# Performance work log

Measured on AMD Instinct MI355X. Metric: run time of the kernel, lower is better.

The kernel has to match this reference:

```python
import jax, jax.numpy as jnp
import numpy as np

N = 50000      # nodes per graph
E = 1600000    # edges per graph
D_IN = 128
D_HID = 128
D_OUT = 128
D_GF = 128
N_LAYERS = 3   # input->hid, hid->hid (hidden_layer=1), hid->out


def setup_inputs() -> dict:
    key = jax.random.key(0)
    ks = jax.random.split(key, 24)
    inp = {
        "feat_p": jax.random.normal(ks[0], (N, D_IN), jnp.float32),
        "src_p": jax.random.randint(ks[1], (E,), 0, N, jnp.int32),
        "dst_p": jax.random.randint(ks[2], (E,), 0, N, jnp.int32),
        "feat_s": jax.random.normal(ks[3], (N, D_IN), jnp.float32),
        "src_s": jax.random.randint(ks[4], (E,), 0, N, jnp.int32),
        "dst_s": jax.random.randint(ks[5], (E,), 0, N, jnp.int32),
    }
    dims = [(D_IN, D_HID), (D_HID, D_HID), (D_HID, D_OUT)]
    for i, (di, do) in enumerate(dims):
        inp[f"W{i}"] = jax.random.normal(ks[6 + 2 * i], (di, do), jnp.float32) * 0.05
        inp[f"b{i}"] = jnp.zeros((do,), jnp.float32)
    inp["Wr"] = jax.random.normal(ks[14], (D_OUT, D_GF), jnp.float32) * 0.05
    inp["br"] = jnp.zeros((D_GF,), jnp.float32)
    inp["Wm1"] = jax.random.normal(ks[15], (2 * D_GF, D_GF), jnp.float32) * 0.05
    inp["bm1"] = jnp.zeros((D_GF,), jnp.float32)
    inp["Wm2"] = jax.random.normal(ks[16], (D_GF, 1), jnp.float32) * 0.05
    inp["bm2"] = jnp.zeros((1,), jnp.float32)
    return inp


def _gcn_stack(feat, src, dst, layers):
    """Stacked GCN: mean over incoming messages, then linear.
    NOTE: the original SingleGCN never applies its ReLU (bug preserved)."""
    n = feat.shape[0]
    deg = jax.ops.segment_sum(jnp.ones_like(src, feat.dtype), dst, num_segments=n)
    inv_deg = (1.0 / jnp.maximum(deg, 1.0))[:, None]  # [N,1]
    h = feat
    for W, b in layers:
        msg = h[src]                                           # [E,d] gather
        agg = jax.ops.segment_sum(msg, dst, num_segments=n)    # [N,d] scatter-add
        h = (agg * inv_deg) @ W + b                            # mean + linear
    return h


def reference(feat_p, src_p, dst_p, feat_s, src_s, dst_s,
              W0, b0, W1, b1, W2, b2, Wr, br, Wm1, bm1, Wm2, bm2):
    layers = [(W0, b0), (W1, b1), (W2, b2)]
    h_p = _gcn_stack(feat_p, src_p, dst_p, layers)
    h_s = _gcn_stack(feat_s, src_s, dst_s, layers)
    # ReadOut: mean over nodes -> linear -> sigmoid
    g_p = jax.nn.sigmoid(jnp.mean(h_p, axis=0) @ Wr + br)  # [D_GF]
    g_s = jax.nn.sigmoid(jnp.mean(h_s, axis=0) @ Wr + br)
    # Match: concat -> linear -> linear -> sigmoid
    c = jnp.concatenate([g_p, g_s], axis=-1)               # [2*D_GF]
    d = (c @ Wm1 + bm1) @ Wm2 + bm2                        # [1]
    return jax.nn.sigmoid(d)
```

## Files before the change

### kernel.cpp

```cpp
#include <hip/hip_runtime.h>
#include <math.h>

#define D 128
#define BSH 9
#define NPB 512
#define SLOT 128
#define STCAP 6252
#define NBB 256
#define NBKT_MAX 128


__global__ __launch_bounds__(512) void bin_kernel(
        const int* __restrict__ src_p, const int* __restrict__ dst_p,
        const int* __restrict__ src_s, const int* __restrict__ dst_s,
        int* __restrict__ sbins, unsigned short* __restrict__ dbins,
        unsigned* __restrict__ cnt_s, unsigned* __restrict__ cnt_d,
        int E, int nbkt) {
    const int g = blockIdx.y, b = blockIdx.x;
    const int* src = g ? src_s : src_p;
    const int* dst = g ? dst_s : dst_p;
    int* sb = sbins + (size_t)g * nbkt * NBB * SLOT;
    unsigned short* db = dbins + (size_t)g * nbkt * NBB * SLOT;
    unsigned* csp = cnt_s + (size_t)g * nbkt * NBB;
    unsigned* cdp = cnt_d + (size_t)g * nbkt * NBB;

    __shared__ int sstage[STCAP];
    __shared__ unsigned short dstage[STCAP];
    __shared__ unsigned hist_s[NBKT_MAX], hist_d[NBKT_MAX];
    __shared__ unsigned offs_s[NBKT_MAX], offs_d[NBKT_MAX];
    __shared__ unsigned lcur_s[NBKT_MAX], lcur_d[NBKT_MAX];

    const int tid = threadIdx.x;
    const int wv = tid >> 6, lane = tid & 63;
    for (int i = tid; i < NBKT_MAX; i += 512) { hist_s[i] = 0u; hist_d[i] = 0u; }
    __syncthreads();

    const int e0 = b * STCAP;
    const int e1 = min(e0 + STCAP, E);
    const int efull = e0 + ((e1 - e0) & ~3);

    for (int e = e0 + tid * 4; e + 4 <= e1; e += 512 * 4) {
        int4 s4 = *(const int4*)(src + e);
        int4 d4 = *(const int4*)(dst + e);
        atomicAdd(&hist_s[s4.x >> BSH], 1u);
        atomicAdd(&hist_s[s4.y >> BSH], 1u);
        atomicAdd(&hist_s[s4.z >> BSH], 1u);
        atomicAdd(&hist_s[s4.w >> BSH], 1u);
        atomicAdd(&hist_d[d4.x >> BSH], 1u);
        atomicAdd(&hist_d[d4.y >> BSH], 1u);
        atomicAdd(&hist_d[d4.z >> BSH], 1u);
        atomicAdd(&hist_d[d4.w >> BSH], 1u);
    }
    for (int e = efull + tid; e < e1; e += 512) {
        atomicAdd(&hist_s[src[e] >> BSH], 1u);
        atomicAdd(&hist_d[dst[e] >> BSH], 1u);
    }
    __syncthreads();

    if (wv == 0 || wv == 1) {
        const unsigned* h = (wv == 0) ? hist_s : hist_d;
        unsigned* o = (wv == 0) ? offs_s : offs_d;
        unsigned* lc = (wv == 0) ? lcur_s : lcur_d;
        unsigned a = (2 * lane < nbkt) ? h[2 * lane] : 0u;
        unsigned bb = (2 * lane + 1 < nbkt) ? h[2 * lane + 1] : 0u;
        unsigned v = a + bb;
        for (int d2 = 1; d2 < 64; d2 <<= 1) {
            unsigned t = __shfl_up(v, d2);
            if (lane >= d2) v += t;
        }
        unsigned ex = v - (a + bb);
        if (2 * lane < nbkt) { o[2 * lane] = ex; lc[2 * lane] = ex; }
        if (2 * lane + 1 < nbkt) { o[2 * lane + 1] = ex + a; lc[2 * lane + 1] = ex + a; }
    }
    __syncthreads();

    for (int e = e0 + tid * 4; e + 4 <= e1; e += 512 * 4) {
        int4 s4 = *(const int4*)(src + e);
        int4 d4 = *(const int4*)(dst + e);
        int sv[4] = {s4.x, s4.y, s4.z, s4.w};
        int dv[4] = {d4.x, d4.y, d4.z, d4.w};
        #pragma unroll
        for (int k = 0; k < 4; ++k) {
            unsigned p = atomicAdd(&lcur_s[sv[k] >> BSH], 1u);
            sstage[p] = ((sv[k] & (NPB - 1)) << 17) | dv[k];
            unsigned pd = atomicAdd(&lcur_d[dv[k] >> BSH], 1u);
            dstage[pd] = (unsigned short)(dv[k] & (NPB - 1));
        }
    }
    for (int e = efull + tid; e < e1; e += 512) {
        int s = src[e], d2 = dst[e];
        unsigned p = atomicAdd(&lcur_s[s >> BSH], 1u);
        sstage[p] = ((s & (NPB - 1)) << 17) | d2;
        unsigned pd = atomicAdd(&lcur_d[d2 >> BSH], 1u);
        dstage[pd] = (unsigned short)(d2 & (NPB - 1));
    }
    __syncthreads();

    for (int q = wv; q < nbkt; q += 8) {
        unsigned cs = min(hist_s[q], (unsigned)SLOT);
        unsigned os = offs_s[q];
        int* dp = sb + ((size_t)q * NBB + b) * SLOT;
        for (unsigned i = lane; i < cs; i += 64) dp[i] = sstage[os + i];
        unsigned cd = min(hist_d[q], (unsigned)SLOT);
        unsigned od = offs_d[q];
        unsigned short* ddp = db + ((size_t)q * NBB + b) * SLOT;
        for (unsigned i = lane; i < cd; i += 64) ddp[i] = dstage[od + i];
        if (lane == 0) { csp[q * NBB + b] = cs; cdp[q * NBB + b] = cd; }
    }
}

__global__ __launch_bounds__(512) void deg_inv(
        const unsigned short* __restrict__ dbins, const unsigned* __restrict__ cnt_d,
        float* __restrict__ inv, float* __restrict__ zbase, int zcount,
        int N, int nbkt) {
    const int q = blockIdx.x, g = blockIdx.y;
    const int tid = threadIdx.x, wv = tid >> 6;
    if (q == 0 && g == 0)
        for (int i = tid; i < zcount; i += 512) zbase[i] = 0.f;
    const unsigned short* dq = dbins + ((size_t)g * nbkt + q) * NBB * SLOT;
    const unsigned* cq = cnt_d + (size_t)g * nbkt * NBB + (size_t)q * NBB;
    __shared__ float bl[8][NPB];
    __shared__ unsigned lcnt[NBB];
    if (tid < NBB) lcnt[tid] = cq[tid];
    for (int i = tid; i < 8 * NPB; i += 512) ((float*)bl)[i] = 0.f;
    __syncthreads();
    float* mybl = bl[wv];
    const ushort4* d4 = (const ushort4*)dq;
    for (int i = tid; i < NBB * (SLOT / 4); i += 512) {
        int lim = (int)lcnt[i >> 5] - ((i & 31) << 2);
        if (lim <= 0) continue;
        ushort4 v = d4[i];
        atomicAdd(&mybl[v.x], 1.f);
        if (lim > 1) atomicAdd(&mybl[v.y], 1.f);
        if (lim > 2) atomicAdd(&mybl[v.z], 1.f);
        if (lim > 3) atomicAdd(&mybl[v.w], 1.f);
    }
    __syncthreads();
    float t = 0.f;
    #pragma unroll
    for (int r = 0; r < 8; ++r) t += bl[r][tid];
    int node = q * NPB + tid;
    if (node < N) inv[(size_t)g * N + node] = 1.0f / fmaxf(t, 1.0f);
}

__global__ __launch_bounds__(512) void prop_scan(
        const int* __restrict__ sbins, const unsigned* __restrict__ cnt_s,
        const float* __restrict__ w, const float* __restrict__ inv,
        float* __restrict__ out_w,
        const float* __restrict__ feat_p, const float* __restrict__ feat_s,
        float* __restrict__ fpart2, float* __restrict__ sums, int s_idx,
        int N, int nbkt, float scale) {
    const int q = blockIdx.x, g = blockIdx.y;
    const int* sq = sbins + ((size_t)g * nbkt + q) * NBB * SLOT;
    const unsigned* cq = cnt_s + (size_t)g * nbkt * NBB + (size_t)q * NBB;
    const float* wg = w + (size_t)g * N;
    const int tid = threadIdx.x, wv = tid >> 6;
    __shared__ float bl[8][NPB];
    __shared__ unsigned lcnt[NBB];
    __shared__ float red[NPB];
    if (tid < NBB) lcnt[tid] = cq[tid];
    for (int i = tid; i < 8 * NPB; i += 512) ((float*)bl)[i] = 0.f;
    __syncthreads();
    float* mybl = bl[wv];
    const int4* s4 = (const int4*)sq;
    for (int i = tid; i < NBB * (SLOT / 4); i += 512) {
        int lim = (int)lcnt[i >> 5] - ((i & 31) << 2);
        if (lim <= 0) continue;
        int4 v = s4[i];
        int iy = (lim > 1) ? (v.y & 0x1FFFF) : 0;
        int iz = (lim > 2) ? (v.z & 0x1FFFF) : 0;
        int iw = (lim > 3) ? (v.w & 0x1FFFF) : 0;
        float a = wg[v.x & 0x1FFFF];
        float b2 = wg[iy];
        float c2 = wg[iz];
        float d2 = wg[iw];
        atomicAdd(&mybl[((unsigned)v.x) >> 17], a);
        if (lim > 1) atomicAdd(&mybl[((unsigned)v.y) >> 17], b2);
        if (lim > 2) atomicAdd(&mybl[((unsigned)v.z) >> 17], c2);
        if (lim > 3) atomicAdd(&mybl[((unsigned)v.w) >> 17], d2);
    }
    __syncthreads();
    float t = 0.f;
    #pragma unroll
    for (int r = 0; r < 8; ++r) t += bl[r][tid];
    const float u = t * scale;
    const int node = q * NPB + tid;
    const bool valid = node < N;
    if (valid && out_w) {
        size_t off = (size_t)g * N + node;
        out_w[off] = u * inv[off];
    }
    if (sums) {
        red[tid] = valid ? u : 0.f;
        __syncthreads();
        for (int st = 256; st > 0; st >>= 1) {
            if (tid < st) red[tid] += red[tid + st];
            __syncthreads();
        }
        if (tid == 0 && red[0] != 0.f) atomicAdd(&sums[g * 2 + s_idx], red[0]);
    }
    if (fpart2) {
        red[tid] = valid ? u : 0.f;
        __syncthreads();
        const float* feat = g ? feat_s : feat_p;
        const int j = tid & 127, rg = tid >> 7;
        const int base = q * NPB;
        const int rmax = min(NPB, N - base);
        float acc = 0.f;
        const int rend = min((rg + 1) * 128, rmax);
        for (int r = rg * 128; r < rend; ++r)
            acc += red[r] * feat[(size_t)(base + r) * D + j];
        ((float*)bl)[rg * 128 + j] = acc;
        __syncthreads();
        if (rg == 0) {
            float tot = ((float*)bl)[j] + ((float*)bl)[128 + j] +
                        ((float*)bl)[256 + j] + ((float*)bl)[384 + j];
            atomicAdd(&fpart2[((size_t)g * 16 + (q & 15)) * D + j], tot);
        }
    }
}

__global__ __launch_bounds__(512) void final_kernel(
        const float* __restrict__ fpart2,
        const float* __restrict__ sums,
        const float* __restrict__ W0, const float* __restrict__ b0,
        const float* __restrict__ W1, const float* __restrict__ b1,
        const float* __restrict__ W2, const float* __restrict__ b2,
        const float* __restrict__ Wr, const float* __restrict__ br,
        const float* __restrict__ Wm1, const float* __restrict__ bm1,
        const float* __restrict__ Wm2, const float* __restrict__ bm2,
        float* __restrict__ out) {
    __shared__ float x[128];
    __shared__ float part[4][128];
    __shared__ float rvec[256];
    __shared__ float Avec[128], Bvec[128];
    __shared__ float gv[256];
    const int tid = threadIdx.x;
    const int j = tid & 127;
    const int h = tid >> 7;

    auto mv128 = [&](const float* __restrict__ W, float* __restrict__ buf) {
        float p = 0.f;
        const float* Wp = W + (size_t)(h * 32) * 128 + j;
        #pragma unroll
        for (int i = 0; i < 32; ++i) p += buf[h * 32 + i] * Wp[(size_t)i * 128];
        part[h][j] = p;
        __syncthreads();
        if (h == 0) buf[j] = part[0][j] + part[1][j] + part[2][j] + part[3][j];
        __syncthreads();
    };

    if (tid < 256) {
        int g = tid >> 7;
        const float* fp = fpart2 + (size_t)g * 2048 + (tid & 127);
        float rv = 0.f;
        #pragma unroll
        for (int b = 0; b < 16; ++b) rv += fp[(size_t)b * 128];
        rvec[tid] = rv;
    }
    __syncthreads();

    if (tid < 128) x[tid] = b0[tid];
    __syncthreads();
    mv128(W1, x);
    mv128(W2, x);
    if (tid < 128) Avec[tid] = x[tid];
    __syncthreads();
    if (tid < 128) x[tid] = b1[tid];
    __syncthreads();
    mv128(W2, x);
    if (tid < 128) Bvec[tid] = x[tid];
    __syncthreads();

    for (int g = 0; g < 2; ++g) {
        const float s1 = sums[g * 2 + 0];
        const float s2 = sums[g * 2 + 1];
        if (tid < 128) x[tid] = rvec[g * 128 + tid];
        __syncthreads();
        mv128(W0, x);
        mv128(W1, x);
        mv128(W2, x);
        if (tid < 128) x[tid] += s2 * Avec[tid] + s1 * Bvec[tid] + b2[tid];
        __syncthreads();
        mv128(Wr, x);
        if (tid < 128) gv[g * 128 + tid] = 1.0f / (1.0f + expf(-(x[tid] + br[tid])));
        __syncthreads();
    }

    {
        float p = 0.f;
        const float* Wp = Wm1 + (size_t)(h * 64) * 128 + j;
        #pragma unroll
        for (int i = 0; i < 64; ++i) p += gv[h * 64 + i] * Wp[(size_t)i * 128];
        part[h][j] = p;
        __syncthreads();
        if (h == 0)
            part[0][j] = (part[0][j] + part[1][j] + part[2][j] + part[3][j] + bm1[j]) * Wm2[j];
        __syncthreads();
        if (tid < 64) part[0][tid] += part[0][tid + 64];
        __syncthreads();
        if (tid < 32) part[0][tid] += part[0][tid + 32];
        __syncthreads();
        if (tid < 16) part[0][tid] += part[0][tid + 16];
        __syncthreads();
        if (tid < 8) part[0][tid] += part[0][tid + 8];
        __syncthreads();
        if (tid < 4) part[0][tid] += part[0][tid + 4];
        __syncthreads();
        if (tid < 2) part[0][tid] += part[0][tid + 2];
        __syncthreads();
        if (tid == 0) out[0] = 1.0f / (1.0f + expf(-(part[0][0] + part[0][1] + bm2[0])));
    }
}

extern "C" void kernel_launch(void* const* d_in, const int* in_sizes, int n_in,
                              void* d_out, int out_size, void* d_ws, size_t ws_size,
                              hipStream_t stream) {
    const float* feat_p = (const float*)d_in[0];
    const int*   src_p  = (const int*)d_in[1];
    const int*   dst_p  = (const int*)d_in[2];
    const float* feat_s = (const float*)d_in[3];
    const int*   src_s  = (const int*)d_in[4];
    const int*   dst_s  = (const int*)d_in[5];
    const float* W0 = (const float*)d_in[6];
    const float* b0 = (const float*)d_in[7];
    const float* W1 = (const float*)d_in[8];
    const float* b1 = (const float*)d_in[9];
    const float* W2 = (const float*)d_in[10];
    const float* b2 = (const float*)d_in[11];
    const float* Wr = (const float*)d_in[12];
    const float* br = (const float*)d_in[13];
    const float* Wm1 = (const float*)d_in[14];
    const float* bm1 = (const float*)d_in[15];
    const float* Wm2 = (const float*)d_in[16];
    const float* bm2 = (const float*)d_in[17];
    float* out = (float*)d_out;

    const int N = in_sizes[0] / D;
    const int E = in_sizes[1];
    const int N2 = 2 * N;
    const int nbkt = (N + NPB - 1) >> BSH;

    float* ws     = (float*)d_ws;
    float* sums   = ws;
    float* fpart2 = ws + 16;
    float* inv    = fpart2 + 2 * 16 * 128;
    float* w1     = inv + N2;
    float* w2     = w1 + N2;
    unsigned* cnt_s = (unsigned*)(w2 + N2);
    unsigned* cnt_d = cnt_s + (size_t)2 * nbkt * NBB;
    int* sbins    = (int*)(cnt_d + (size_t)2 * nbkt * NBB);
    unsigned short* dbins = (unsigned short*)(sbins + (size_t)2 * nbkt * NBB * SLOT);

    const float u0 = 1.0f / (float)N;
    const int zcount = 16 + 2 * 16 * 128;

    bin_kernel<<<dim3(NBB, 2), 512, 0, stream>>>(src_p, dst_p, src_s, dst_s,
                                                 sbins, dbins, cnt_s, cnt_d,
                                                 E, nbkt);

    deg_inv<<<dim3(nbkt, 2), 512, 0, stream>>>(dbins, cnt_d, inv, ws, zcount,
                                               N, nbkt);

    prop_scan<<<dim3(nbkt, 2), 512, 0, stream>>>(sbins, cnt_s, inv, inv, w1,
                                                 nullptr, nullptr, nullptr,
                                                 sums, 0, N, nbkt, u0);
    prop_scan<<<dim3(nbkt, 2), 512, 0, stream>>>(sbins, cnt_s, w1, inv, w2,
                                                 nullptr, nullptr, nullptr,
                                                 sums, 1, N, nbkt, 1.0f);
    prop_scan<<<dim3(nbkt, 2), 512, 0, stream>>>(sbins, cnt_s, w2, inv, nullptr,
                                                 feat_p, feat_s, fpart2,
                                                 nullptr, 0, N, nbkt, 1.0f);

    final_kernel<<<1, 512, 0, stream>>>(fpart2, sums, W0, b0, W1, b1, W2, b2,
                                        Wr, br, Wm1, bm1, Wm2, bm2, out);
}
```

Baseline: 317.2 us.

## Split per-bucket degree and propagation scans into sub-block partials plus combine kernels

The degree-count and scalar-propagation scans ran with only about 196 blocks (nbkt × 2). They are now split eight ways along the source-block dimension, giving about 1568 blocks of 256 threads. Each block writes per-node partial sums to a workspace buffer, and separate combine kernels sum the partials, apply inv-degree, reduce the sums and do the feature-weighted accumulation. The feature pass is now spread over twice as many blocks. This should fill the GPU's compute units better, at the cost of extra launches and partials traffic through global memory.

```diff
diff --git a/kernel.cpp b/kernel.cpp
--- a/kernel.cpp
+++ b/kernel.cpp
@@ -8,6 +8,8 @@
 #define STCAP 6252
 #define NBB 256
 #define NBKT_MAX 128
+#define SB 8
+#define CPS (NBB / SB)
 
 
 __global__ __launch_bounds__(512) void bin_kernel(
@@ -109,24 +111,22 @@
     }
 }
 
-__global__ __launch_bounds__(512) void deg_inv(
+__global__ __launch_bounds__(256) void deg_part(
         const unsigned short* __restrict__ dbins, const unsigned* __restrict__ cnt_d,
-        float* __restrict__ inv, float* __restrict__ zbase, int zcount,
-        int N, int nbkt) {
-    const int q = blockIdx.x, g = blockIdx.y;
+        float* __restrict__ partials, int nbkt) {
+    const int s = blockIdx.x, q = blockIdx.y, g = blockIdx.z;
+    const unsigned short* dq = dbins + ((size_t)(g * nbkt + q) * NBB + s * CPS) * SLOT;
+    const unsigned* cq = cnt_d + (size_t)(g * nbkt + q) * NBB + s * CPS;
     const int tid = threadIdx.x, wv = tid >> 6;
-    if (q == 0 && g == 0)
-        for (int i = tid; i < zcount; i += 512) zbase[i] = 0.f;
-    const unsigned short* dq = dbins + ((size_t)g * nbkt + q) * NBB * SLOT;
-    const unsigned* cq = cnt_d + (size_t)g * nbkt * NBB + (size_t)q * NBB;
-    __shared__ float bl[8][NPB];
-    __shared__ unsigned lcnt[NBB];
-    if (tid < NBB) lcnt[tid] = cq[tid];
-    for (int i = tid; i < 8 * NPB; i += 512) ((float*)bl)[i] = 0.f;
+    __shared__ float bl[4][NPB];
+    __shared__ unsigned lcnt[CPS];
+    if (tid < CPS) lcnt[tid] = cq[tid];
+    for (int i = tid; i < 4 * NPB; i += 256) ((float*)bl)[i] = 0.f;
     __syncthreads();
     float* mybl = bl[wv];
     const ushort4* d4 = (const ushort4*)dq;
-    for (int i = tid; i < NBB * (SLOT / 4); i += 512) {
+    const int total = CPS * (SLOT / 4);
+    for (int i = tid; i < total; i += 256) {
         int lim = (int)lcnt[i >> 5] - ((i & 31) << 2);
         if (lim <= 0) continue;
         ushort4 v = d4[i];
@@ -136,34 +136,44 @@
         if (lim > 3) atomicAdd(&mybl[v.w], 1.f);
     }
     __syncthreads();
+    float* pp = partials + (((size_t)(g * nbkt + q)) * SB + s) * NPB;
+    for (int i = tid; i < NPB; i += 256)
+        pp[i] = bl[0][i] + bl[1][i] + bl[2][i] + bl[3][i];
+}
+
+__global__ __launch_bounds__(512) void deg_combine(
+        const float* __restrict__ partials, float* __restrict__ inv,
+        float* __restrict__ zbase, int zcount, int N, int nbkt) {
+    const int q = blockIdx.x, g = blockIdx.y;
+    const int tid = threadIdx.x;
+    if (q == 0 && g == 0)
+        for (int i = tid; i < zcount; i += 512) zbase[i] = 0.f;
+    const float* pp = partials + ((size_t)(g * nbkt + q)) * SB * NPB;
     float t = 0.f;
     #pragma unroll
-    for (int r = 0; r < 8; ++r) t += bl[r][tid];
-    int node = q * NPB + tid;
+    for (int s = 0; s < SB; ++s) t += pp[s * NPB + tid];
+    const int node = q * NPB + tid;
     if (node < N) inv[(size_t)g * N + node] = 1.0f / fmaxf(t, 1.0f);
 }
 
-__global__ __launch_bounds__(512) void prop_scan(
+__global__ __launch_bounds__(256) void part_scan(
         const int* __restrict__ sbins, const unsigned* __restrict__ cnt_s,
-        const float* __restrict__ w, const float* __restrict__ inv,
-        float* __restrict__ out_w,
-        const float* __restrict__ feat_p, const float* __restrict__ feat_s,
-        float* __restrict__ fpart2, float* __restrict__ sums, int s_idx,
-        int N, int nbkt, float scale) {
-    const int q = blockIdx.x, g = blockIdx.y;
-    const int* sq = sbins + ((size_t)g * nbkt + q) * NBB * SLOT;
-    const unsigned* cq = cnt_s + (size_t)g * nbkt * NBB + (size_t)q * NBB;
+        const float* __restrict__ w, float* __restrict__ partials,
+        int N, int nbkt) {
+    const int s = blockIdx.x, q = blockIdx.y, g = blockIdx.z;
+    const int* sq = sbins + ((size_t)(g * nbkt + q) * NBB + s * CPS) * SLOT;
+    const unsigned* cq = cnt_s + (size_t)(g * nbkt + q) * NBB + s * CPS;
     const float* wg = w + (size_t)g * N;
     const int tid = threadIdx.x, wv = tid >> 6;
-    __shared__ float bl[8][NPB];
-    __shared__ unsigned lcnt[NBB];
-    __shared__ float red[NPB];
-    if (tid < NBB) lcnt[tid] = cq[tid];
-    for (int i = tid; i < 8 * NPB; i += 512) ((float*)bl)[i] = 0.f;
+    __shared__ float bl[4][NPB];
+    __shared__ unsigned lcnt[CPS];
+    if (tid < CPS) lcnt[tid] = cq[tid];
+    for (int i = tid; i < 4 * NPB; i += 256) ((float*)bl)[i] = 0.f;
     __syncthreads();
     float* mybl = bl[wv];
     const int4* s4 = (const int4*)sq;
-    for (int i = tid; i < NBB * (SLOT / 4); i += 512) {
+    const int total = CPS * (SLOT / 4);
+    for (int i = tid; i < total; i += 256) {
         int lim = (int)lcnt[i >> 5] - ((i & 31) << 2);
         if (lim <= 0) continue;
         int4 v = s4[i];
@@ -180,43 +190,70 @@
         if (lim > 3) atomicAdd(&mybl[((unsigned)v.w) >> 17], d2);
     }
     __syncthreads();
+    float* pp = partials + (((size_t)(g * nbkt + q)) * SB + s) * NPB;
+    for (int i = tid; i < NPB; i += 256)
+        pp[i] = bl[0][i] + bl[1][i] + bl[2][i] + bl[3][i];
+}
+
+__global__ __launch_bounds__(512) void prop_combine(
+        const float* __restrict__ partials, const float* __restrict__ inv,
+        float* __restrict__ out_w, float* __restrict__ sums, int s_idx,
+        int N, int nbkt, float scale) {
+    const int q = blockIdx.x, g = blockIdx.y;
+    const int tid = threadIdx.x;
+    const float* pp = partials + ((size_t)(g * nbkt + q)) * SB * NPB;
     float t = 0.f;
     #pragma unroll
-    for (int r = 0; r < 8; ++r) t += bl[r][tid];
+    for (int s = 0; s < SB; ++s) t += pp[s * NPB + tid];
     const float u = t * scale;
     const int node = q * NPB + tid;
     const bool valid = node < N;
-    if (valid && out_w) {
+    if (valid) {
         size_t off = (size_t)g * N + node;
         out_w[off] = u * inv[off];
     }
-    if (sums) {
-        red[tid] = valid ? u : 0.f;
-        __syncthreads();
-        for (int st = 256; st > 0; st >>= 1) {
-            if (tid < st) red[tid] += red[tid + st];
-            __syncthreads();
-        }
-        if (tid == 0 && red[0] != 0.f) atomicAdd(&sums[g * 2 + s_idx], red[0]);
-    }
-    if (fpart2) {
-        red[tid] = valid ? u : 0.f;
-        __syncthreads();
-        const float* feat = g ? feat_s : feat_p;
-        const int j = tid & 127, rg = tid >> 7;
-        const int base = q * NPB;
-        const int rmax = min(NPB, N - base);
-        float acc = 0.f;
-        const int rend = min((rg + 1) * 128, rmax);
-        for (int r = rg * 128; r < rend; ++r)
-            acc += red[r] * feat[(size_t)(base + r) * D + j];
-        ((float*)bl)[rg * 128 + j] = acc;
-        __syncthreads();
-        if (rg == 0) {
-            float tot = ((float*)bl)[j] + ((float*)bl)[128 + j] +
-                        ((float*)bl)[256 + j] + ((float*)bl)[384 + j];
+    __shared__ float red[NPB];
+    red[tid] = valid ? u : 0.f;
+    __syncthreads();
+    for (int st = 256; st > 0; st >>= 1) {
+        if (tid < st) red[tid] += red[tid + st];
+        __syncthreads();
+    }
+    if (tid == 0 && red[0] != 0.f) atomicAdd(&sums[g * 2 + s_idx], red[0]);
+}
+
+__global__ __launch_bounds__(512) void feat_combine(
+        const float* __restrict__ partials,
+        const float* __restrict__ feat_p, const float* __restrict__ feat_s,
+        float* __restrict__ fpart2, int N, int nbkt) {
+    const int r = blockIdx.x, q = blockIdx.y, g = blockIdx.z;
+    const int tid = threadIdx.x;
+    __shared__ float red[256];
+    __shared__ float accb[512];
+    const float* pp = partials + ((size_t)(g * nbkt + q)) * SB * NPB + r * 256;
+    const int base = q * NPB + r * 256;
+    if (tid < 256) {
+        float t = 0.f;
+        #pragma unroll
+        for (int s = 0; s < SB; ++s) t += pp[s * NPB + tid];
+        red[tid] = (base + tid < N) ? t : 0.f;
+    }
+    __syncthreads();
+    const float* feat = g ? feat_s : feat_p;
+    const int j = tid & 127, rg = tid >> 7;
+    int rmax = N - base;
+    rmax = (rmax < 0) ? 0 : ((rmax > 256) ? 256 : rmax);
+    const int rstart = rg * 64;
+    const int rend = min(rstart + 64, rmax);
+    float acc = 0.f;
+    for (int row = rstart; row < rend; ++row)
+        acc += red[row] * feat[(size_t)(base + row) * D + j];
+    accb[rg * 128 + j] = acc;
+    __syncthreads();
+    if (rg == 0) {
+        float tot = accb[j] + accb[128 + j] + accb[256 + j] + accb[384 + j];
+        if (tot != 0.f)
             atomicAdd(&fpart2[((size_t)g * 16 + (q & 15)) * D + j], tot);
-        }
     }
 }
 
@@ -347,7 +384,8 @@
     float* inv    = fpart2 + 2 * 16 * 128;
     float* w1     = inv + N2;
     float* w2     = w1 + N2;
-    unsigned* cnt_s = (unsigned*)(w2 + N2);
+    float* partials = w2 + N2;
+    unsigned* cnt_s = (unsigned*)(partials + (size_t)2 * nbkt * SB * NPB);
     unsigned* cnt_d = cnt_s + (size_t)2 * nbkt * NBB;
     int* sbins    = (int*)(cnt_d + (size_t)2 * nbkt * NBB);
     unsigned short* dbins = (unsigned short*)(sbins + (size_t)2 * nbkt * NBB * SLOT);
@@ -359,18 +397,24 @@
                                                  sbins, dbins, cnt_s, cnt_d,
                                                  E, nbkt);
 
-    deg_inv<<<dim3(nbkt, 2), 512, 0, stream>>>(dbins, cnt_d, inv, ws, zcount,
-                                               N, nbkt);
-
-    prop_scan<<<dim3(nbkt, 2), 512, 0, stream>>>(sbins, cnt_s, inv, inv, w1,
-                                                 nullptr, nullptr, nullptr,
-                                                 sums, 0, N, nbkt, u0);
-    prop_scan<<<dim3(nbkt, 2), 512, 0, stream>>>(sbins, cnt_s, w1, inv, w2,
-                                                 nullptr, nullptr, nullptr,
-                                                 sums, 1, N, nbkt, 1.0f);
-    prop_scan<<<dim3(nbkt, 2), 512, 0, stream>>>(sbins, cnt_s, w2, inv, nullptr,
-                                                 feat_p, feat_s, fpart2,
-                                                 nullptr, 0, N, nbkt, 1.0f);
+    deg_part<<<dim3(SB, nbkt, 2), 256, 0, stream>>>(dbins, cnt_d, partials, nbkt);
+    deg_combine<<<dim3(nbkt, 2), 512, 0, stream>>>(partials, inv, ws, zcount,
+                                                   N, nbkt);
+
+    part_scan<<<dim3(SB, nbkt, 2), 256, 0, stream>>>(sbins, cnt_s, inv,
+                                                     partials, N, nbkt);
+    prop_combine<<<dim3(nbkt, 2), 512, 0, stream>>>(partials, inv, w1,
+                                                    sums, 0, N, nbkt, u0);
+
+    part_scan<<<dim3(SB, nbkt, 2), 256, 0, stream>>>(sbins, cnt_s, w1,
+                                                     partials, N, nbkt);
+    prop_combine<<<dim3(nbkt, 2), 512, 0, stream>>>(partials, inv, w2,
+                                                    sums, 1, N, nbkt, 1.0f);
+
+    part_scan<<<dim3(SB, nbkt, 2), 256, 0, stream>>>(sbins, cnt_s, w2,
+                                                     partials, N, nbkt);
+    feat_combine<<<dim3(2, nbkt, 2), 512, 0, stream>>>(partials, feat_p, feat_s,
+                                                       fpart2, N, nbkt);
 
     final_kernel<<<1, 512, 0, stream>>>(fpart2, sums, W0, b0, W1, b1, W2, b2,
                                         Wr, br, Wm1, bm1, Wm2, bm2, out);
```

Measured after the change: 300.8 us. -5.2%, faster.
